# Optimization experiments

Hardware: AMD Instinct MI355X
Metric: run time of the kernel (lower is better)

Reference implementation:

```python
import jax, jax.numpy as jnp
import numpy as np

EPS = 1e-5

def _layernorm(x, gamma, beta):
    mu = jnp.mean(x, axis=-1, keepdims=True)
    var = jnp.var(x, axis=-1, keepdims=True)
    return (x - mu) * jax.lax.rsqrt(var + EPS) * gamma + beta

def setup_inputs() -> dict:
    key = jax.random.key(0)
    ks = jax.random.split(key, 8)
    B, N, c_z, c_h = 1, 384, 128, 128
    s_z = 1.0 / np.sqrt(c_z)
    s_h = 1.0 / np.sqrt(c_h)
    return {
        "z_ij": jax.random.normal(ks[0], (B, N, N, c_z), dtype=jnp.float32),
        "ln_in_g": jnp.ones((c_z,), jnp.float32),
        "ln_in_b": jnp.zeros((c_z,), jnp.float32),
        "ln_out_g": jnp.ones((c_h,), jnp.float32),
        "ln_out_b": jnp.zeros((c_h,), jnp.float32),
        "Wa1": jax.random.uniform(ks[1], (c_h, c_z), jnp.float32, -s_z, s_z),
        "Wa2": jax.random.uniform(ks[2], (c_h, c_z), jnp.float32, -s_z, s_z),
        "Wb1": jax.random.uniform(ks[3], (c_h, c_z), jnp.float32, -s_z, s_z),
        "Wb2": jax.random.uniform(ks[4], (c_h, c_z), jnp.float32, -s_z, s_z),
        "Wg": jax.random.uniform(ks[5], (c_z, c_z), jnp.float32, -s_z, s_z),
        "Wout": jax.random.uniform(ks[6], (c_z, c_h), jnp.float32, -s_h, s_h),
    }

def reference(z_ij, ln_in_g, ln_in_b, ln_out_g, ln_out_b, Wa1, Wa2, Wb1, Wb2, Wg, Wout):
    # Algorithm 12: triangular multiplicative update, "outgoing" edges
    z = _layernorm(z_ij, ln_in_g, ln_in_b)              # [B,N,N,c_z]
    a = jax.nn.sigmoid(z @ Wa1.T) * (z @ Wa2.T)         # [B,N,N,c_h]
    b = jax.nn.sigmoid(z @ Wb1.T) * (z @ Wb2.T)         # [B,N,N,c_h]
    g = jax.nn.sigmoid(z @ Wg.T)                        # [B,N,N,c_z]
    s = jnp.einsum('bikd,bjkd->bijd', a, b)             # pairwise contraction over k
    return g * (_layernorm(s, ln_out_g, ln_out_b) @ Wout.T)
```

## Files before the change

kernel.cpp:

```cpp
#include <hip/hip_runtime.h>
#include <stdint.h>

#define N 384
#define NR (N*N)
#define PL (NR + 64)
#define C 128
#define WSZ 16384

typedef unsigned short ushort_t;
typedef __attribute__((ext_vector_type(8))) _Float16 f16x8;
typedef __attribute__((ext_vector_type(4))) float f32x4;

__device__ __forceinline__ ushort_t f2h(float f) {
  union { _Float16 h; ushort_t u; } v; v.h = (_Float16)f; return v.u;
}
__device__ __forceinline__ void unpack8h(uint4 q, float f[8]) {
  union { uint4 q; _Float16 h[8]; } v; v.q = q;
#pragma unroll
  for (int e = 0; e < 8; ++e) f[e] = (float)v.h[e];
}
__device__ __forceinline__ uint4 pack8h(const float f[8]) {
  union { uint4 q; _Float16 h[8]; } v;
#pragma unroll
  for (int e = 0; e < 8; ++e) v.h[e] = (_Float16)f[e];
  return v.q;
}

__device__ __forceinline__ float bf2f(ushort_t u) {
  union { unsigned int i; float f; } v; v.i = ((unsigned int)u) << 16; return v.f;
}
__device__ __forceinline__ ushort_t f2bf(float f) {
  union { float f; unsigned int i; } v; v.f = f;
  unsigned int u = v.i + 0x7FFF + ((v.i >> 16) & 1);
  return (ushort_t)(u >> 16);
}
__device__ __forceinline__ void unpack8bf(uint4 q, float f[8]) {
  const unsigned int* w = (const unsigned int*)&q;
#pragma unroll
  for (int e = 0; e < 4; ++e) {
    f[2*e]   = bf2f((ushort_t)(w[e] & 0xffffu));
    f[2*e+1] = bf2f((ushort_t)(w[e] >> 16));
  }
}
__device__ __forceinline__ uint4 pack8bf(const float f[8]) {
  uint4 q;
  unsigned int* w = (unsigned int*)&q;
#pragma unroll
  for (int e = 0; e < 4; ++e)
    w[e] = (unsigned int)f2bf(f[2*e]) | ((unsigned int)f2bf(f[2*e+1]) << 16);
  return q;
}

__device__ __forceinline__ float sigmoidf_(float x) {
  return __builtin_amdgcn_rcpf(1.0f + __expf(-x));
}

__device__ __forceinline__ void load8f(const void* p, size_t idx, int isf32, float f[8]) {
  if (isf32) {
    const float* q = (const float*)p + idx;
    const float4 a = ((const float4*)q)[0];
    const float4 b = ((const float4*)q)[1];
    f[0]=a.x; f[1]=a.y; f[2]=a.z; f[3]=a.w;
    f[4]=b.x; f[5]=b.y; f[6]=b.z; f[7]=b.w;
  } else {
    unpack8bf(*(const uint4*)((const ushort_t*)p + idx), f);
  }
}
__device__ __forceinline__ void store8(void* p, size_t idx, int isf32, const float f[8]) {
  if (isf32) {
    float* q = (float*)p + idx;
    ((float4*)q)[0] = make_float4(f[0], f[1], f[2], f[3]);
    ((float4*)q)[1] = make_float4(f[4], f[5], f[6], f[7]);
  } else {
    *(uint4*)((ushort_t*)p + idx) = pack8bf(f);
  }
}
__device__ __forceinline__ void store1(void* p, size_t idx, int isf32, float v) {
  if (isf32) ((float*)p)[idx] = v;
  else       ((ushort_t*)p)[idx] = f2bf(v);
}

__global__ void kprep(const unsigned int* __restrict__ zw,
                      const void* __restrict__ Wa1, const void* __restrict__ Wa2,
                      const void* __restrict__ Wb1, const void* __restrict__ Wb2,
                      const void* __restrict__ Wg,  const void* __restrict__ Wout,
                      ushort_t* __restrict__ wp, int* __restrict__ flag)
{
  const int t = threadIdx.x;
  __shared__ int cnt[4];
  {
    unsigned int u = zw[t];
    int e = (u >> 23) & 0xFF;
    int sane = (e >= 87 && e <= 132) ? 1 : 0;
    unsigned long long b = __ballot(sane);
    if ((t & 63) == 0) cnt[t >> 6] = __popcll(b);
  }
  __syncthreads();
  const int isf32 = ((cnt[0] + cnt[1] + cnt[2] + cnt[3]) >= 128) ? 1 : 0;
  if (blockIdx.x == 0 && t == 0) flag[0] = isf32;

  const void* src;
  switch (blockIdx.x) {
    case 0: src = Wa1; break;
    case 1: src = Wa2; break;
    case 2: src = Wb1; break;
    case 3: src = Wb2; break;
    case 4: src = Wg;  break;
    default: src = Wout; break;
  }
  ushort_t* dst = wp + (size_t)blockIdx.x * WSZ;
  for (int c = t; c < 2048; c += 256) {
    int ks = c >> 9, nf = (c >> 6) & 7, lane = c & 63;
    int quad = lane >> 4, l16 = lane & 15;
    size_t sidx = (size_t)(nf*16 + l16)*128 + ks*32 + quad*8;
    float f[8]; load8f(src, sidx, isf32, f);
    *(uint4*)(dst + (size_t)c*8) = pack8h(f);
  }
}

__global__ __launch_bounds__(256, 4)
void k1a(const void* __restrict__ z, const void* __restrict__ gin,
         const void* __restrict__ bin, ushort_t* __restrict__ zn,
         const int* __restrict__ flag)
{
  const int isf32 = *flag;
  const int tid = blockIdx.x * 256 + threadIdx.x;
  const int r = tid >> 2, h = tid & 3;
  float x[4][8];
  float sum = 0.f, sq = 0.f;
#pragma unroll
  for (int j = 0; j < 4; ++j) {
    load8f(z, (size_t)r*C + h*32 + j*8, isf32, x[j]);
#pragma unroll
    for (int e = 0; e < 8; ++e) { sum += x[j][e]; sq += x[j][e]*x[j][e]; }
  }
  sum += __shfl_xor(sum, 1); sum += __shfl_xor(sum, 2);
  sq  += __shfl_xor(sq, 1);  sq  += __shfl_xor(sq, 2);
  const float mu = sum * 0.0078125f;
  const float rstd = rsqrtf(sq * 0.0078125f - mu*mu + 1e-5f);
#pragma unroll
  for (int j = 0; j < 4; ++j) {
    float ga[8], be[8];
    load8f(gin, (size_t)(h*32 + j*8), isf32, ga);
    load8f(bin, (size_t)(h*32 + j*8), isf32, be);
    float f[8];
#pragma unroll
    for (int e = 0; e < 8; ++e) f[e] = (x[j][e] - mu) * rstd * ga[e] + be[e];
    *(uint4*)(zn + (size_t)r*C + h*32 + j*8) = pack8h(f);
  }
}

__global__ __launch_bounds__(256, 2)
void k1b(const ushort_t* __restrict__ zn, const ushort_t* __restrict__ wp,
         ushort_t* __restrict__ a_t, ushort_t* __restrict__ b_t,
         void* __restrict__ gout, ushort_t* __restrict__ g_t, int gIsWs,
         const int* __restrict__ flag)
{
  __shared__ ushort_t tb[128*72];
  const int t = threadIdx.x;
  const int isf32 = *flag;
  const int wave = t >> 6, lane = t & 63;
  const int quad = lane >> 4, l16 = lane & 15;
  const int rg = wave >> 1, ch = wave & 1;
  const int R0 = blockIdx.x * 64;
  const f32x4 z4 = {0.f, 0.f, 0.f, 0.f};

  f16x8 af[2][4];
#pragma unroll
  for (int mf = 0; mf < 2; ++mf) {
    const int row = R0 + rg*32 + mf*16 + l16;
#pragma unroll
    for (int ks = 0; ks < 4; ++ks)
      af[mf][ks] = *(const f16x8*)(zn + (size_t)row*C + ks*32 + quad*8);
  }

  auto pair = [&](const ushort_t* W1p, const ushort_t* W2p, ushort_t* dst) {
#pragma unroll 1
    for (int nh = 0; nh < 2; ++nh) {
      f32x4 a1[2][2], a2[2][2];
#pragma unroll
      for (int mf = 0; mf < 2; ++mf)
#pragma unroll
        for (int nn = 0; nn < 2; ++nn) { a1[mf][nn] = z4; a2[mf][nn] = z4; }
#pragma unroll
      for (int ks = 0; ks < 4; ++ks)
#pragma unroll
        for (int nn = 0; nn < 2; ++nn) {
          const size_t foff = (size_t)((ks*8 + ch*4 + nh*2 + nn)*64 + lane) * 8;
          f16x8 b1 = *(const f16x8*)(W1p + foff);
          f16x8 b2 = *(const f16x8*)(W2p + foff);
#pragma unroll
          for (int mf = 0; mf < 2; ++mf) {
            a1[mf][nn] = __builtin_amdgcn_mfma_f32_16x16x32_f16(af[mf][ks], b1, a1[mf][nn], 0, 0, 0);
            a2[mf][nn] = __builtin_amdgcn_mfma_f32_16x16x32_f16(af[mf][ks], b2, a2[mf][nn], 0, 0, 0);
          }
        }
#pragma unroll
      for (int mf = 0; mf < 2; ++mf)
#pragma unroll
        for (int nn = 0; nn < 2; ++nn)
#pragma unroll
          for (int r = 0; r < 4; ++r) {
            int rowl = rg*32 + mf*16 + quad*4 + r;
            int col  = ch*64 + (nh*2 + nn)*16 + l16;
            tb[col*72 + rowl] = f2h(a2[mf][nn][r] * sigmoidf_(a1[mf][nn][r]));
          }
    }
    asm volatile("s_waitcnt lgkmcnt(0)" ::: "memory");
    __builtin_amdgcn_s_barrier();
#pragma unroll
    for (int i = 0; i < 4; ++i) {
      int cid = t + i*256, dl = cid >> 3, rc = cid & 7;
      uint4 v = *(const uint4*)(tb + dl*72 + rc*8);
      *(uint4*)(dst + (size_t)dl*PL + R0 + rc*8) = v;
    }
    asm volatile("" ::: "memory");
    __builtin_amdgcn_s_barrier();
  };
  pair(wp + 0*WSZ, wp + 1*WSZ, a_t);
  pair(wp + 2*WSZ, wp + 3*WSZ, b_t);

  {
    const ushort_t* Wgp = wp + 4*WSZ;
    f32x4 ag[2][4];
#pragma unroll
    for (int mf = 0; mf < 2; ++mf)
#pragma unroll
      for (int nf = 0; nf < 4; ++nf) ag[mf][nf] = z4;
#pragma unroll
    for (int ks = 0; ks < 4; ++ks)
#pragma unroll
      for (int nf = 0; nf < 4; ++nf) {
        const size_t foff = (size_t)((ks*8 + ch*4 + nf)*64 + lane) * 8;
        f16x8 b = *(const f16x8*)(Wgp + foff);
#pragma unroll
        for (int mf = 0; mf < 2; ++mf)
          ag[mf][nf] = __builtin_amdgcn_mfma_f32_16x16x32_f16(af[mf][ks], b, ag[mf][nf], 0, 0, 0);
      }
#pragma unroll
    for (int mf = 0; mf < 2; ++mf)
#pragma unroll
      for (int nf = 0; nf < 4; ++nf)
#pragma unroll
        for (int r = 0; r < 4; ++r) {
          int row = R0 + rg*32 + mf*16 + quad*4 + r;
          int col = ch*64 + nf*16 + l16;
          float v = sigmoidf_(ag[mf][nf][r]);
          size_t idx = (size_t)row*C + col;
          if (gIsWs) g_t[idx] = f2h(v);
          else       store1(gout, idx, isf32, v);
        }
  }
}

__global__ __launch_bounds__(256, 3)
void k2(const ushort_t* __restrict__ a_t, const ushort_t* __restrict__ b_t,
        ushort_t* __restrict__ s_t)
{
  __shared__ ushort_t As[128*64];
  __shared__ ushort_t Bs[128*64];
  const int t = threadIdx.x;
  const int wave = t >> 6, lane = t & 63;
  const int quad = lane >> 4, l16 = lane & 15;
  const int wm = wave >> 1, wn = wave & 1;
  const int lin = blockIdx.x;
  const int xcd = lin & 7, slot = lin >> 3;
  const int d = xcd + 8*(slot/9);
  const int tile = slot - (slot/9)*9;
  const int i0 = (tile/3) * 128, j0 = (tile%3) * 128;
  const size_t dbase = (size_t)d * PL;

  f32x4 acc[4][4];
  const f32x4 z4 = {0.f, 0.f, 0.f, 0.f};
#pragma unroll
  for (int mf = 0; mf < 4; ++mf)
#pragma unroll
    for (int nf = 0; nf < 4; ++nf) acc[mf][nf] = z4;

  uint4 va[4], vb[4];
#pragma unroll
  for (int j = 0; j < 4; ++j) {
    int cid = t + j*256, row = cid >> 3, c = cid & 7;
    va[j] = *(const uint4*)(a_t + dbase + (size_t)(i0 + row)*N + c*8);
    vb[j] = *(const uint4*)(b_t + dbase + (size_t)(j0 + row)*N + c*8);
  }

  for (int kt = 0; kt < 6; ++kt) {
#pragma unroll
    for (int j = 0; j < 4; ++j) {
      int cid = t + j*256, row = cid >> 3, c = cid & 7;
      int p = c ^ (row & 7);
      *(uint4*)(As + row*64 + p*8) = va[j];
      *(uint4*)(Bs + row*64 + p*8) = vb[j];
    }
    if (kt < 5) {
#pragma unroll
      for (int j = 0; j < 4; ++j) {
        int cid = t + j*256, row = cid >> 3, c = cid & 7;
        va[j] = *(const uint4*)(a_t + dbase + (size_t)(i0 + row)*N + (kt+1)*64 + c*8);
        vb[j] = *(const uint4*)(b_t + dbase + (size_t)(j0 + row)*N + (kt+1)*64 + c*8);
      }
    }
    asm volatile("s_waitcnt lgkmcnt(0)" ::: "memory");
    __builtin_amdgcn_s_barrier();

#pragma unroll
    for (int ks = 0; ks < 2; ++ks) {
      f16x8 afr[4], bfr[4];
#pragma unroll
      for (int f = 0; f < 4; ++f) {
        int ra = wm*64 + f*16 + l16;
        int pa = (ks*4 + quad) ^ (ra & 7);
        afr[f] = *(const f16x8*)(As + ra*64 + pa*8);
        int rb = wn*64 + f*16 + l16;
        int pb = (ks*4 + quad) ^ (rb & 7);
        bfr[f] = *(const f16x8*)(Bs + rb*64 + pb*8);
      }
#pragma unroll
      for (int mf = 0; mf < 4; ++mf)
#pragma unroll
        for (int nf = 0; nf < 4; ++nf)
          acc[mf][nf] = __builtin_amdgcn_mfma_f32_16x16x32_f16(afr[mf], bfr[nf], acc[mf][nf], 0, 0, 0);
    }
    asm volatile("" ::: "memory");
    __builtin_amdgcn_s_barrier();
  }
#pragma unroll
  for (int mf = 0; mf < 4; ++mf)
#pragma unroll
    for (int nf = 0; nf < 4; ++nf)
#pragma unroll
      for (int r = 0; r < 4; ++r) {
        int row = wm*64 + mf*16 + quad*4 + r;
        int col = wn*64 + nf*16 + l16;
        s_t[dbase + (size_t)(i0 + row)*N + j0 + col] = f2h(acc[mf][nf][r]);
      }
}

__global__ __launch_bounds__(256, 2)
void k3(const ushort_t* __restrict__ s_t, const void* __restrict__ gno,
        const void* __restrict__ bno, const ushort_t* __restrict__ wp,
        void* __restrict__ io, const ushort_t* __restrict__ g_t, int gIsWs,
        const int* __restrict__ flag)
{
  __shared__ ushort_t ss[128*136];
  const int t = threadIdx.x;
  const int isf32 = *flag;
  const int wave = t >> 6, lane = t & 63;
  const int quad = lane >> 4, l16 = lane & 15;
  const int R0 = blockIdx.x * 128;
  const ushort_t* Woutp = wp + 5*WSZ;

  {
    const int dg = t >> 4, rg = t & 15;
    const int d0 = dg * 8;
    uint4 v[8];
#pragma unroll
    for (int dd = 0; dd < 8; ++dd)
      v[dd] = *(const uint4*)(s_t + (size_t)(d0 + dd)*PL + R0 + rg*8);
    const ushort_t* sv = (const ushort_t*)v;
#pragma unroll
    for (int rr0 = 0; rr0 < 8; ++rr0) {
      int rr = (rr0 + (t & 7)) & 7;
      ushort_t w[8];
#pragma unroll
      for (int dd = 0; dd < 8; ++dd) w[dd] = sv[dd*8 + rr];
      *(uint4*)(ss + (rg*8 + rr)*136 + d0) = *(const uint4*)w;
    }
  }
  asm volatile("s_waitcnt lgkmcnt(0)" ::: "memory");
  __builtin_amdgcn_s_barrier();

  {
    const int r = t >> 1, h = t & 1;
    float sum = 0.f, sq = 0.f;
#pragma unroll
    for (int j = 0; j < 8; ++j) {
      uint4 q = *(const uint4*)(ss + r*136 + (h*8 + j)*8);
      float f[8]; unpack8h(q, f);
#pragma unroll
      for (int e = 0; e < 8; ++e) { sum += f[e]; sq += f[e]*f[e]; }
    }
    sum += __shfl_xor(sum, 1);
    sq  += __shfl_xor(sq, 1);
    const float mu = sum * 0.0078125f;
    const float rstd = rsqrtf(sq * 0.0078125f - mu*mu + 1e-5f);
#pragma unroll
    for (int j = 0; j < 8; ++j) {
      const int g = h*8 + j;
      uint4 q = *(const uint4*)(ss + r*136 + g*8);
      float f[8], gm[8], bt[8];
      unpack8h(q, f);
      load8f(gno, (size_t)g*8, isf32, gm);
      load8f(bno, (size_t)g*8, isf32, bt);
#pragma unroll
      for (int e = 0; e < 8; ++e) f[e] = (f[e] - mu) * rstd * gm[e] + bt[e];
      *(uint4*)(ss + r*136 + g*8) = pack8h(f);
    }
  }
  asm volatile("s_waitcnt lgkmcnt(0)" ::: "memory");
  __builtin_amdgcn_s_barrier();

  f16x8 afr[2][4];
#pragma unroll
  for (int ks = 0; ks < 4; ++ks)
#pragma unroll
    for (int mf = 0; mf < 2; ++mf) {
      int row = wave*32 + mf*16 + l16;
      afr[mf][ks] = *(const f16x8*)(ss + row*136 + (ks*4 + quad)*8);
    }
  asm volatile("s_waitcnt lgkmcnt(0)" ::: "memory");
  __builtin_amdgcn_s_barrier();

  const f32x4 z4 = {0.f, 0.f, 0.f, 0.f};
#pragma unroll 1
  for (int nh = 0; nh < 2; ++nh) {
    f32x4 acc[2][4];
#pragma unroll
    for (int mf = 0; mf < 2; ++mf)
#pragma unroll
      for (int nn = 0; nn < 4; ++nn) acc[mf][nn] = z4;
#pragma unroll
    for (int ks = 0; ks < 4; ++ks)
#pragma unroll
      for (int nn = 0; nn < 4; ++nn) {
        size_t foff = (size_t)(((ks*8 + nh*4 + nn)*64 + lane)) * 8;
        f16x8 b = *(const f16x8*)(Woutp + foff);
#pragma unroll
        for (int mf = 0; mf < 2; ++mf)
          acc[mf][nn] = __builtin_amdgcn_mfma_f32_16x16x32_f16(afr[mf][ks], b, acc[mf][nn], 0, 0, 0);
      }
#pragma unroll
    for (int mf = 0; mf < 2; ++mf)
#pragma unroll
      for (int nn = 0; nn < 4; ++nn)
#pragma unroll
        for (int r = 0; r < 4; ++r) {
          int row = wave*32 + mf*16 + quad*4 + r;
          int col = (nh*4 + nn)*16 + l16;
          ss[row*136 + col] = f2h(acc[mf][nn][r]);
        }
  }
  asm volatile("s_waitcnt lgkmcnt(0)" ::: "memory");
  __builtin_amdgcn_s_barrier();

#pragma unroll
  for (int i = 0; i < 8; ++i) {
    int cid = t + i*256;
    int row = cid >> 4, ch = cid & 15;
    size_t idx = (size_t)(R0 + row)*C + ch*8;
    float gf[8], hf[8], of[8];
    if (gIsWs) unpack8h(*(const uint4*)(g_t + idx), gf);
    else       load8f(io, idx, isf32, gf);
    unpack8h(*(const uint4*)(ss + row*136 + ch*8), hf);
#pragma unroll
    for (int e = 0; e < 8; ++e) of[e] = gf[e] * hf[e];
    store8(io, idx, isf32, of);
  }
}

extern "C" void kernel_launch(void* const* d_in, const int* in_sizes, int n_in,
                              void* d_out, int out_size, void* d_ws, size_t ws_size,
                              hipStream_t stream) {
  (void)in_sizes; (void)n_in; (void)out_size;
  const void* z    = d_in[0];
  const void* gin  = d_in[1];
  const void* bin  = d_in[2];
  const void* gno  = d_in[3];
  const void* bno  = d_in[4];
  const void* Wa1  = d_in[5];
  const void* Wa2  = d_in[6];
  const void* Wb1  = d_in[7];
  const void* Wb2  = d_in[8];
  const void* Wg   = d_in[9];
  const void* Wout = d_in[10];

  const size_t plane = (size_t)C * PL;
  int* flag     = (int*)d_ws;
  ushort_t* wp  = (ushort_t*)((char*)d_ws + 256);
  ushort_t* a_t = wp + (size_t)6*WSZ;
  ushort_t* b_t = a_t + plane;
  ushort_t* s_t = b_t + plane;
  ushort_t* g_t = s_t + plane;
  size_t need_g = 256 + (size_t)6*WSZ*2 + (3*plane + (size_t)NR*C)*2;
  int gIsWs = (ws_size >= need_g) ? 1 : 0;

  ushort_t* zn = s_t;

  kprep<<<6, 256, 0, stream>>>((const unsigned int*)z, Wa1, Wa2, Wb1, Wb2, Wg, Wout, wp, flag);
  k1a<<<NR*4/256, 256, 0, stream>>>(z, gin, bin, zn, flag);
  k1b<<<NR/64, 256, 0, stream>>>(zn, wp, a_t, b_t, d_out, g_t, gIsWs, flag);
  k2<<<1152, 256, 0, stream>>>(a_t, b_t, s_t);
  k3<<<NR/128, 256, 0, stream>>>(s_t, gno, bno, wp, d_out, g_t, gIsWs, flag);
}
```

Before: 327.0 us.

## Merge weight prep into layernorm kernel and halve k3 row tile

The weight-packing kernel and the input layernorm kernel become one launch: each block recomputes the dtype flag locally, and the first six blocks pack weights while the rest normalize rows. This removes one launch and the dependency on a flag written by a previous kernel. k3 now processes 64 rows per block instead of 128, which doubles the grid. The output layernorm is applied while building the MFMA A fragments, using per-row mean and rstd kept in shared memory, instead of a separate normalize-and-write-back pass through LDS. Each block now issues more Wout fragment loads relative to the work it does.

```diff
diff --git a/kernel.cpp b/kernel.cpp
--- a/kernel.cpp
+++ b/kernel.cpp
@@ -80,11 +80,14 @@
   else       ((ushort_t*)p)[idx] = f2bf(v);
 }
 
-__global__ void kprep(const unsigned int* __restrict__ zw,
-                      const void* __restrict__ Wa1, const void* __restrict__ Wa2,
-                      const void* __restrict__ Wb1, const void* __restrict__ Wb2,
-                      const void* __restrict__ Wg,  const void* __restrict__ Wout,
-                      ushort_t* __restrict__ wp, int* __restrict__ flag)
+__global__ __launch_bounds__(256, 4)
+void k0(const unsigned int* __restrict__ zw, const void* __restrict__ z,
+        const void* __restrict__ gin, const void* __restrict__ bin,
+        const void* __restrict__ Wa1, const void* __restrict__ Wa2,
+        const void* __restrict__ Wb1, const void* __restrict__ Wb2,
+        const void* __restrict__ Wg,  const void* __restrict__ Wout,
+        ushort_t* __restrict__ wp, ushort_t* __restrict__ zn,
+        int* __restrict__ flag)
 {
   const int t = threadIdx.x;
   __shared__ int cnt[4];
@@ -97,34 +100,31 @@
   }
   __syncthreads();
   const int isf32 = ((cnt[0] + cnt[1] + cnt[2] + cnt[3]) >= 128) ? 1 : 0;
-  if (blockIdx.x == 0 && t == 0) flag[0] = isf32;
-
-  const void* src;
-  switch (blockIdx.x) {
-    case 0: src = Wa1; break;
-    case 1: src = Wa2; break;
-    case 2: src = Wb1; break;
-    case 3: src = Wb2; break;
-    case 4: src = Wg;  break;
-    default: src = Wout; break;
-  }
-  ushort_t* dst = wp + (size_t)blockIdx.x * WSZ;
-  for (int c = t; c < 2048; c += 256) {
-    int ks = c >> 9, nf = (c >> 6) & 7, lane = c & 63;
-    int quad = lane >> 4, l16 = lane & 15;
-    size_t sidx = (size_t)(nf*16 + l16)*128 + ks*32 + quad*8;
-    float f[8]; load8f(src, sidx, isf32, f);
-    *(uint4*)(dst + (size_t)c*8) = pack8h(f);
-  }
-}
-
-__global__ __launch_bounds__(256, 4)
-void k1a(const void* __restrict__ z, const void* __restrict__ gin,
-         const void* __restrict__ bin, ushort_t* __restrict__ zn,
-         const int* __restrict__ flag)
-{
-  const int isf32 = *flag;
-  const int tid = blockIdx.x * 256 + threadIdx.x;
+  const int bid = blockIdx.x;
+  if (bid == 0 && t == 0) flag[0] = isf32;
+
+  if (bid < 6) {
+    const void* src;
+    switch (bid) {
+      case 0: src = Wa1; break;
+      case 1: src = Wa2; break;
+      case 2: src = Wb1; break;
+      case 3: src = Wb2; break;
+      case 4: src = Wg;  break;
+      default: src = Wout; break;
+    }
+    ushort_t* dst = wp + (size_t)bid * WSZ;
+    for (int c = t; c < 2048; c += 256) {
+      int ks = c >> 9, nf = (c >> 6) & 7, lane = c & 63;
+      int quad = lane >> 4, l16 = lane & 15;
+      size_t sidx = (size_t)(nf*16 + l16)*128 + ks*32 + quad*8;
+      float f[8]; load8f(src, sidx, isf32, f);
+      *(uint4*)(dst + (size_t)c*8) = pack8h(f);
+    }
+    return;
+  }
+
+  const int tid = (bid - 6) * 256 + t;
   const int r = tid >> 2, h = tid & 3;
   float x[4][8];
   float sum = 0.f, sq = 0.f;
@@ -343,109 +343,107 @@
         void* __restrict__ io, const ushort_t* __restrict__ g_t, int gIsWs,
         const int* __restrict__ flag)
 {
-  __shared__ ushort_t ss[128*136];
+  __shared__ ushort_t ss[64*136];
+  __shared__ float muA[64];
+  __shared__ float rsA[64];
   const int t = threadIdx.x;
   const int isf32 = *flag;
   const int wave = t >> 6, lane = t & 63;
   const int quad = lane >> 4, l16 = lane & 15;
-  const int R0 = blockIdx.x * 128;
+  const int R0 = blockIdx.x * 64;
   const ushort_t* Woutp = wp + 5*WSZ;
 
   {
-    const int dg = t >> 4, rg = t & 15;
-    const int d0 = dg * 8;
-    uint4 v[8];
-#pragma unroll
-    for (int dd = 0; dd < 8; ++dd)
+    const int dg = t >> 3, rg = t & 7;
+    const int d0 = dg * 4;
+    uint4 v[4];
+#pragma unroll
+    for (int dd = 0; dd < 4; ++dd)
       v[dd] = *(const uint4*)(s_t + (size_t)(d0 + dd)*PL + R0 + rg*8);
     const ushort_t* sv = (const ushort_t*)v;
 #pragma unroll
     for (int rr0 = 0; rr0 < 8; ++rr0) {
       int rr = (rr0 + (t & 7)) & 7;
-      ushort_t w[8];
-#pragma unroll
-      for (int dd = 0; dd < 8; ++dd) w[dd] = sv[dd*8 + rr];
-      *(uint4*)(ss + (rg*8 + rr)*136 + d0) = *(const uint4*)w;
+      alignas(8) ushort_t w[4];
+#pragma unroll
+      for (int dd = 0; dd < 4; ++dd) w[dd] = sv[dd*8 + rr];
+      *(uint2*)(ss + (rg*8 + rr)*136 + d0) = *(const uint2*)w;
     }
   }
   asm volatile("s_waitcnt lgkmcnt(0)" ::: "memory");
   __builtin_amdgcn_s_barrier();
 
   {
-    const int r = t >> 1, h = t & 1;
+    const int r = t >> 2, h = t & 3;
     float sum = 0.f, sq = 0.f;
 #pragma unroll
-    for (int j = 0; j < 8; ++j) {
-      uint4 q = *(const uint4*)(ss + r*136 + (h*8 + j)*8);
+    for (int j = 0; j < 4; ++j) {
+      uint4 q = *(const uint4*)(ss + r*136 + h*32 + j*8);
       float f[8]; unpack8h(q, f);
 #pragma unroll
       for (int e = 0; e < 8; ++e) { sum += f[e]; sq += f[e]*f[e]; }
     }
-    sum += __shfl_xor(sum, 1);
-    sq  += __shfl_xor(sq, 1);
-    const float mu = sum * 0.0078125f;
-    const float rstd = rsqrtf(sq * 0.0078125f - mu*mu + 1e-5f);
-#pragma unroll
-    for (int j = 0; j < 8; ++j) {
-      const int g = h*8 + j;
-      uint4 q = *(const uint4*)(ss + r*136 + g*8);
-      float f[8], gm[8], bt[8];
-      unpack8h(q, f);
-      load8f(gno, (size_t)g*8, isf32, gm);
-      load8f(bno, (size_t)g*8, isf32, bt);
-#pragma unroll
-      for (int e = 0; e < 8; ++e) f[e] = (f[e] - mu) * rstd * gm[e] + bt[e];
-      *(uint4*)(ss + r*136 + g*8) = pack8h(f);
+    sum += __shfl_xor(sum, 1); sum += __shfl_xor(sum, 2);
+    sq  += __shfl_xor(sq, 1);  sq  += __shfl_xor(sq, 2);
+    if (h == 0) {
+      const float mu = sum * 0.0078125f;
+      muA[r] = mu;
+      rsA[r] = rsqrtf(sq * 0.0078125f - mu*mu + 1e-5f);
     }
   }
   asm volatile("s_waitcnt lgkmcnt(0)" ::: "memory");
   __builtin_amdgcn_s_barrier();
 
-  f16x8 afr[2][4];
-#pragma unroll
-  for (int ks = 0; ks < 4; ++ks)
-#pragma unroll
-    for (int mf = 0; mf < 2; ++mf) {
-      int row = wave*32 + mf*16 + l16;
-      afr[mf][ks] = *(const f16x8*)(ss + row*136 + (ks*4 + quad)*8);
-    }
+  f16x8 afr[4];
+  {
+    const int frow = wave*16 + l16;
+    const float mu_r = muA[frow];
+    const float rs_r = rsA[frow];
+#pragma unroll
+    for (int ks = 0; ks < 4; ++ks) {
+      uint4 raw = *(const uint4*)(ss + frow*136 + (ks*4 + quad)*8);
+      float f[8], ga[8], be[8];
+      unpack8h(raw, f);
+      load8f(gno, (size_t)(ks*32 + quad*8), isf32, ga);
+      load8f(bno, (size_t)(ks*32 + quad*8), isf32, be);
+      union { alignas(16) _Float16 h[8]; f16x8 v; } u;
+#pragma unroll
+      for (int e = 0; e < 8; ++e)
+        u.h[e] = (_Float16)((f[e] - mu_r) * rs_r * ga[e] + be[e]);
+      afr[ks] = u.v;
+    }
+  }
   asm volatile("s_waitcnt lgkmcnt(0)" ::: "memory");
   __builtin_amdgcn_s_barrier();
 
   const f32x4 z4 = {0.f, 0.f, 0.f, 0.f};
 #pragma unroll 1
   for (int nh = 0; nh < 2; ++nh) {
-    f32x4 acc[2][4];
-#pragma unroll
-    for (int mf = 0; mf < 2; ++mf)
-#pragma unroll
-      for (int nn = 0; nn < 4; ++nn) acc[mf][nn] = z4;
+    f32x4 acc[4];
+#pragma unroll
+    for (int nn = 0; nn < 4; ++nn) acc[nn] = z4;
 #pragma unroll
     for (int ks = 0; ks < 4; ++ks)
 #pragma unroll
       for (int nn = 0; nn < 4; ++nn) {
         size_t foff = (size_t)(((ks*8 + nh*4 + nn)*64 + lane)) * 8;
         f16x8 b = *(const f16x8*)(Woutp + foff);
-#pragma unroll
-        for (int mf = 0; mf < 2; ++mf)
-          acc[mf][nn] = __builtin_amdgcn_mfma_f32_16x16x32_f16(afr[mf][ks], b, acc[mf][nn], 0, 0, 0);
-      }
-#pragma unroll
-    for (int mf = 0; mf < 2; ++mf)
-#pragma unroll
-      for (int nn = 0; nn < 4; ++nn)
-#pragma unroll
-        for (int r = 0; r < 4; ++r) {
-          int row = wave*32 + mf*16 + quad*4 + r;
-          int col = (nh*4 + nn)*16 + l16;
-          ss[row*136 + col] = f2h(acc[mf][nn][r]);
-        }
+        acc[nn] = __builtin_amdgcn_mfma_f32_16x16x32_f16(afr[ks], b, acc[nn], 0, 0, 0);
+      }
+#pragma unroll
+    for (int nn = 0; nn < 4; ++nn)
+#pragma unroll
+      for (int r = 0; r < 4; ++r) {
+        int row = wave*16 + quad*4 + r;
+        int col = (nh*4 + nn)*16 + l16;
+        ss[row*136 + col] = f2h(acc[nn][r]);
+      }
   }
   asm volatile("s_waitcnt lgkmcnt(0)" ::: "memory");
   __builtin_amdgcn_s_barrier();
 
 #pragma unroll
-  for (int i = 0; i < 8; ++i) {
+  for (int i = 0; i < 4; ++i) {
     int cid = t + i*256;
     int row = cid >> 4, ch = cid & 15;
     size_t idx = (size_t)(R0 + row)*C + ch*8;
@@ -487,9 +485,9 @@
 
   ushort_t* zn = s_t;
 
-  kprep<<<6, 256, 0, stream>>>((const unsigned int*)z, Wa1, Wa2, Wb1, Wb2, Wg, Wout, wp, flag);
-  k1a<<<NR*4/256, 256, 0, stream>>>(z, gin, bin, zn, flag);
+  k0<<<6 + NR*4/256, 256, 0, stream>>>((const unsigned int*)z, z, gin, bin,
+                                       Wa1, Wa2, Wb1, Wb2, Wg, Wout, wp, zn, flag);
   k1b<<<NR/64, 256, 0, stream>>>(zn, wp, a_t, b_t, d_out, g_t, gIsWs, flag);
   k2<<<1152, 256, 0, stream>>>(a_t, b_t, s_t);
-  k3<<<NR/128, 256, 0, stream>>>(s_t, gno, bno, wp, d_out, g_t, gIsWs, flag);
-}
+  k3<<<NR/64, 256, 0, stream>>>(s_t, gno, bno, wp, d_out, g_t, gIsWs, flag);
+}
```

New measurement: 297.5 us. -9.0%, faster.
